# Kernel tuning notes

Measured on AMD Instinct MI355X. Metric: run time of the kernel, lower is better.

The kernel has to match this reference:

```python
import jax, jax.numpy as jnp
import numpy as np

B, C, H, W = 16, 64, 128, 128
E = 8          # number of experts
TOPK = 2       # num_expert (top-k routing)


def setup_inputs() -> dict:
    key = jax.random.key(0)
    ks = jax.random.split(key, 8)
    s = 1.0 / np.sqrt(C)
    x = jax.random.normal(ks[0], (B, C, H, W), dtype=jnp.float32)
    k = jax.random.normal(ks[1], (B, C, 1, 1), dtype=jnp.float32)
    Wg = jax.random.normal(ks[2], (C, E), dtype=jnp.float32) * s
    bg = jnp.zeros((E,), dtype=jnp.float32)
    W1 = jax.random.normal(ks[3], (E, C, C), dtype=jnp.float32) * s  # [E, out, in]
    b1 = jnp.zeros((E, C), dtype=jnp.float32)
    W2 = jax.random.normal(ks[4], (E, C, C), dtype=jnp.float32) * s
    b2 = jnp.zeros((E, C), dtype=jnp.float32)
    return {"x": x, "k": k, "Wg": Wg, "bg": bg, "W1": W1, "b1": b1, "W2": W2, "b2": b2}


def reference(x, k, Wg, bg, W1, b1, W2, b2):
    # --- gate: global avg pool + linear -> [B, E] logits ---
    pooled = x.mean(axis=(2, 3))                              # [B, C]
    logits = pooled @ Wg + bg                                  # [B, E]
    # softmax in fp32 then cast back (matches F.softmax(dtype=torch.float).to(x.dtype))
    weights = jax.nn.softmax(logits.astype(jnp.float32), axis=1).astype(x.dtype)
    topk_w, topk_idx = jax.lax.top_k(weights, TOPK)           # [B, TOPK]
    # scatter top-k weights into dense per-expert mask [B, E]
    mask = jnp.zeros_like(weights).at[jnp.arange(B)[:, None], topk_idx].set(topk_w)
    # --- training branch: run ALL experts, combine with mask ---
    # expert_e(x, k) = W2_e @ gelu((W1_e @ x + b1_e) * k) + b2_e   (1x1 convs)
    h = jnp.einsum('eoc,bchw->ebohw', W1, x) + b1[:, None, :, None, None]
    h = jax.nn.gelu(h * k[None])                               # [E, B, C, H, W]
    y = jnp.einsum('eoc,ebchw->ebohw', W2, h) + b2[:, None, :, None, None]
    out = x + jnp.einsum('ebchw,be->bchw', y, mask)
    return out
```

## Files before the change

kernel.cpp:

```cpp
#include <hip/hip_runtime.h>
#include <hip/hip_bf16.h>


#define BB 16
#define CC 64
#define EE 8
#define HWPX 16384

typedef __bf16 bf16x8 __attribute__((ext_vector_type(8)));
typedef float f32x4 __attribute__((ext_vector_type(4)));

__device__ __forceinline__ unsigned packbf2(float lo, float hi) {
    __bf16 a = (__bf16)lo, b = (__bf16)hi;
    unsigned short ua = __builtin_bit_cast(unsigned short, a);
    unsigned short ub = __builtin_bit_cast(unsigned short, b);
    return ((unsigned)ub << 16) | (unsigned)ua;
}

__device__ __forceinline__ int swz(int px, int d) {
    return px * 32 + ((d & ~3) ^ ((px & 7) << 2)) + (d & 3);
}

__global__ __launch_bounds__(256) void pool_conv_kernel(
    const float* __restrict__ x, float* __restrict__ pooled,
    const float* __restrict__ W1, const float* __restrict__ W2,
    __bf16* __restrict__ W1b, __bf16* __restrict__ W2b) {
    int blk = blockIdx.x;
    if (blk < BB * CC) {
        const float4* p = (const float4*)(x + (size_t)blk * HWPX);
        float s = 0.f;
        for (int i = threadIdx.x; i < HWPX / 4; i += 256) {
            float4 v = p[i];
            s += (v.x + v.y) + (v.z + v.w);
        }
        #pragma unroll
        for (int off = 32; off > 0; off >>= 1) s += __shfl_down(s, off);
        __shared__ float ls[4];
        if ((threadIdx.x & 63) == 0) ls[threadIdx.x >> 6] = s;
        __syncthreads();
        if (threadIdx.x == 0) pooled[blk] = ((ls[0] + ls[1]) + (ls[2] + ls[3])) * (1.0f / (float)HWPX);
    } else {
        int i = (blk - BB * CC) * 256 + threadIdx.x;
        W1b[i] = (__bf16)W1[i];
        W2b[i] = (__bf16)W2[i];
    }
}

__global__ void gate_kernel(const float* __restrict__ pooled,
                            const float* __restrict__ Wg,
                            const float* __restrict__ bg,
                            int* __restrict__ gidx, float* __restrict__ gw) {
    int b = threadIdx.x;
    if (b >= BB) return;
    float logits[EE];
    #pragma unroll
    for (int e = 0; e < EE; ++e) logits[e] = bg[e];
    for (int c = 0; c < CC; ++c) {
        float pv = pooled[b * CC + c];
        #pragma unroll
        for (int e = 0; e < EE; ++e) logits[e] = fmaf(pv, Wg[c * EE + e], logits[e]);
    }
    float m = logits[0];
    #pragma unroll
    for (int e = 1; e < EE; ++e) m = fmaxf(m, logits[e]);
    float w[EE]; float den = 0.f;
    #pragma unroll
    for (int e = 0; e < EE; ++e) { w[e] = expf(logits[e] - m); den += w[e]; }
    float inv = 1.0f / den;
    #pragma unroll
    for (int e = 0; e < EE; ++e) w[e] *= inv;
    int i0 = 0;
    #pragma unroll
    for (int e = 1; e < EE; ++e) if (w[e] > w[i0]) i0 = e;
    int i1 = -1;
    #pragma unroll
    for (int e = 0; e < EE; ++e) {
        if (e == i0) continue;
        if (i1 < 0 || w[e] > w[i1]) i1 = e;
    }
    gidx[b * 2 + 0] = i0; gidx[b * 2 + 1] = i1;
    gw[b * 2 + 0] = w[i0]; gw[b * 2 + 1] = w[i1];
}

__global__ __launch_bounds__(256) void moe_main(
    const float* __restrict__ x, const float* __restrict__ kvec,
    const __bf16* __restrict__ W1b, const float* __restrict__ b1,
    const __bf16* __restrict__ W2b, const float* __restrict__ b2,
    const int* __restrict__ gidx, const float* __restrict__ gw,
    float* __restrict__ out) {

    __shared__ unsigned int lds[2][64 * 32];

    const int blk = blockIdx.x;
    const int b = blk >> 8;
    const int p0 = (blk & 255) << 6;
    const int t = threadIdx.x;
    const int w = t >> 6;
    const int l = t & 63;
    const int g = l >> 4;
    const int l15 = l & 15;

    const int arow = 16 * w + l15;
    const int r0w = 16 * w + 4 * g;

    const int e0 = __builtin_amdgcn_readfirstlane(gidx[b * 2 + 0]);
    const int e1 = __builtin_amdgcn_readfirstlane(gidx[b * 2 + 1]);
    const float wgt0 = gw[b * 2 + 0];
    const float wgt1 = gw[b * 2 + 1];

    bf16x8 a1f[2][2];
    #pragma unroll
    for (int ks = 0; ks < 2; ++ks) {
        a1f[0][ks] = *(const bf16x8*)(W1b + e0 * CC * CC + arow * CC + ks * 32 + g * 8);
        a1f[1][ks] = *(const bf16x8*)(W1b + e1 * CC * CC + arow * CC + ks * 32 + g * 8);
    }
    float b1j[2][4], b2j[2][4], kkj[4];
    #pragma unroll
    for (int j = 0; j < 4; ++j) {
        b1j[0][j] = b1[e0 * CC + r0w + j];
        b1j[1][j] = b1[e1 * CC + r0w + j];
        b2j[0][j] = b2[e0 * CC + r0w + j];
        b2j[1][j] = b2[e1 * CC + r0w + j];
        kkj[j]    = kvec[b * CC + r0w + j];
    }

    {
        const int c0 = (t & 31);
        const int px0 = (t >> 5) * 8;
        const float* r0 = x + ((size_t)(b * CC + c0 * 2)) * HWPX + p0 + px0;
        const float* r1 = r0 + HWPX;
        float4 A0 = *(const float4*)(r0);
        float4 A1 = *(const float4*)(r0 + 4);
        float4 B0 = *(const float4*)(r1);
        float4 B1 = *(const float4*)(r1 + 4);
        float av[8] = {A0.x, A0.y, A0.z, A0.w, A1.x, A1.y, A1.z, A1.w};
        float bv[8] = {B0.x, B0.y, B0.z, B0.w, B1.x, B1.y, B1.z, B1.w};
        #pragma unroll
        for (int i = 0; i < 8; ++i)
            lds[0][swz(px0 + i, c0)] = packbf2(av[i], bv[i]);
    }
    __syncthreads();

    bf16x8 bx[4][2];
    #pragma unroll
    for (int cb = 0; cb < 4; ++cb)
        #pragma unroll
        for (int ks = 0; ks < 2; ++ks)
            bx[cb][ks] = *(const bf16x8*)&lds[0][swz(cb * 16 + l15, ks * 16 + g * 4)];

    const float C1 = -2.302208239f;
    const float C2 = -0.1029434f;

    f32x4 h0[4], h1[4];
    #pragma unroll
    for (int cb = 0; cb < 4; ++cb) {
        h0[cb] = (f32x4){0.f, 0.f, 0.f, 0.f};
        h1[cb] = (f32x4){0.f, 0.f, 0.f, 0.f};
        #pragma unroll
        for (int ks = 0; ks < 2; ++ks) {
            h0[cb] = __builtin_amdgcn_mfma_f32_16x16x32_bf16(a1f[0][ks], bx[cb][ks], h0[cb], 0, 0, 0);
            h1[cb] = __builtin_amdgcn_mfma_f32_16x16x32_bf16(a1f[1][ks], bx[cb][ks], h1[cb], 0, 0, 0);
        }
    }

    uint2 p0k[4], p1k[4];
    #pragma unroll
    for (int cb = 0; cb < 4; ++cb) {
        float hv0[4], hv1[4];
        #pragma unroll
        for (int j = 0; j < 4; ++j) {
            float a0 = h0[cb][j] + b1j[0][j];
            float t0 = a0 * kkj[j];
            float ex0 = __builtin_amdgcn_exp2f(t0 * fmaf(C2, t0 * t0, C1));
            hv0[j] = (t0 * wgt0) * __builtin_amdgcn_rcpf(ex0 + 1.f);
            float a1 = h1[cb][j] + b1j[1][j];
            float t1 = a1 * kkj[j];
            float ex1 = __builtin_amdgcn_exp2f(t1 * fmaf(C2, t1 * t1, C1));
            hv1[j] = (t1 * wgt1) * __builtin_amdgcn_rcpf(ex1 + 1.f);
        }
        p0k[cb].x = packbf2(hv0[0], hv0[1]);
        p0k[cb].y = packbf2(hv0[2], hv0[3]);
        p1k[cb].x = packbf2(hv1[0], hv1[1]);
        p1k[cb].y = packbf2(hv1[2], hv1[3]);
    }

    #pragma unroll
    for (int cb = 0; cb < 4; ++cb)
        *(uint2*)&lds[1][swz(cb * 16 + l15, 8 * w + 2 * g)] = p0k[cb];

    bf16x8 a2f[2][2];
    #pragma unroll
    for (int ks = 0; ks < 2; ++ks) {
        a2f[0][ks] = *(const bf16x8*)(W2b + e0 * CC * CC + arow * CC + ks * 32 + g * 8);
        a2f[1][ks] = *(const bf16x8*)(W2b + e1 * CC * CC + arow * CC + ks * 32 + g * 8);
    }

    __syncthreads();

    #pragma unroll
    for (int cb = 0; cb < 4; ++cb)
        *(uint2*)&lds[0][swz(cb * 16 + l15, 8 * w + 2 * g)] = p1k[cb];

    const float* xbase = x + (size_t)b * CC * HWPX + p0;
    float xp[4][4];
    #pragma unroll
    for (int cb = 0; cb < 4; ++cb)
        #pragma unroll
        for (int j = 0; j < 4; ++j)
            xp[cb][j] = xbase[(size_t)(r0w + j) * HWPX + cb * 16 + l15];

    f32x4 acc2[4];
    #pragma unroll
    for (int cb = 0; cb < 4; ++cb) acc2[cb] = (f32x4){0.f, 0.f, 0.f, 0.f};

    #pragma unroll
    for (int cb = 0; cb < 4; ++cb) {
        #pragma unroll
        for (int ks = 0; ks < 2; ++ks) {
            bf16x8 bh = *(const bf16x8*)&lds[1][swz(cb * 16 + l15, ks * 16 + g * 4)];
            acc2[cb] = __builtin_amdgcn_mfma_f32_16x16x32_bf16(a2f[0][ks], bh, acc2[cb], 0, 0, 0);
        }
    }

    __syncthreads();

    #pragma unroll
    for (int cb = 0; cb < 4; ++cb) {
        #pragma unroll
        for (int ks = 0; ks < 2; ++ks) {
            bf16x8 bh = *(const bf16x8*)&lds[0][swz(cb * 16 + l15, ks * 16 + g * 4)];
            acc2[cb] = __builtin_amdgcn_mfma_f32_16x16x32_bf16(a2f[1][ks], bh, acc2[cb], 0, 0, 0);
        }
    }

    float bsum[4];
    #pragma unroll
    for (int j = 0; j < 4; ++j)
        bsum[j] = fmaf(wgt0, b2j[0][j], wgt1 * b2j[1][j]);

    float* obase = out + (size_t)b * CC * HWPX + p0;
    #pragma unroll
    for (int cb = 0; cb < 4; ++cb) {
        const int col = cb * 16 + l15;
        #pragma unroll
        for (int j = 0; j < 4; ++j) {
            size_t off = (size_t)(r0w + j) * HWPX + col;
            obase[off] = xp[cb][j] + (acc2[cb][j] + bsum[j]);
        }
    }
}

extern "C" void kernel_launch(void* const* d_in, const int* in_sizes, int n_in,
                              void* d_out, int out_size, void* d_ws, size_t ws_size,
                              hipStream_t stream) {
    const float* x  = (const float*)d_in[0];
    const float* k  = (const float*)d_in[1];
    const float* Wg = (const float*)d_in[2];
    const float* bg = (const float*)d_in[3];
    const float* W1 = (const float*)d_in[4];
    const float* b1 = (const float*)d_in[5];
    const float* W2 = (const float*)d_in[6];
    const float* b2 = (const float*)d_in[7];
    float* out = (float*)d_out;

    float*  pooled = (float*)d_ws;
    int*    gidx   = (int*)((char*)d_ws + 4096);
    float*  gw     = (float*)((char*)d_ws + 4096 + 128);
    __bf16* W1b    = (__bf16*)((char*)d_ws + 8192);
    __bf16* W2b    = (__bf16*)((char*)d_ws + 8192 + 65536);

    pool_conv_kernel<<<BB * CC + EE * CC * CC / 256, 256, 0, stream>>>(x, pooled, W1, W2, W1b, W2b);
    gate_kernel<<<1, 64, 0, stream>>>(pooled, Wg, bg, gidx, gw);
    moe_main<<<BB * 256, 256, 0, stream>>>(x, k, W1b, b1, W2b, b2, gidx, gw, out);
}
```

Before: 56.57 us.

## Process four pixel tiles per block with prefetch of next x tile

Each block of moe_main now walks four consecutive 64-pixel tiles instead of one, so the grid shrinks from 4096 to 1024 blocks. Expert weights, biases and k are loaded once per block and reused across the tiles. The next tile's x values are prefetched into registers while the current tile computes. The x tile is now read once per tile (strided per lane) and reused for both the bf16 LDS staging and the residual add, replacing the previous separate vectorized load and reload. The cost is longer-lived registers, more barriers per block, and fewer blocks to hide latency.

New measurement: 51.15 us. 9.6% less time.

```diff
diff --git a/kernel.cpp b/kernel.cpp
--- a/kernel.cpp
+++ b/kernel.cpp
@@ -6,6 +6,7 @@
 #define CC 64
 #define EE 8
 #define HWPX 16384
+#define NT 4
 
 typedef __bf16 bf16x8 __attribute__((ext_vector_type(8)));
 typedef float f32x4 __attribute__((ext_vector_type(4)));
@@ -89,11 +90,12 @@
     const int* __restrict__ gidx, const float* __restrict__ gw,
     float* __restrict__ out) {
 
-    __shared__ unsigned int lds[2][64 * 32];
+    __shared__ unsigned int LA[64 * 32];
+    __shared__ unsigned int LB[64 * 32];
 
     const int blk = blockIdx.x;
-    const int b = blk >> 8;
-    const int p0 = (blk & 255) << 6;
+    const int b = blk >> 6;
+    const int P0 = (blk & 63) << 8;
     const int t = threadIdx.x;
     const int w = t >> 6;
     const int l = t & 63;
@@ -102,150 +104,156 @@
 
     const int arow = 16 * w + l15;
     const int r0w = 16 * w + 4 * g;
+    const int d0 = 8 * w + 2 * g;
 
     const int e0 = __builtin_amdgcn_readfirstlane(gidx[b * 2 + 0]);
     const int e1 = __builtin_amdgcn_readfirstlane(gidx[b * 2 + 1]);
     const float wgt0 = gw[b * 2 + 0];
     const float wgt1 = gw[b * 2 + 1];
 
-    bf16x8 a1f[2][2];
+    const float* xb = x + b * CC * HWPX;
+    float* ob = out + b * CC * HWPX;
+    const int obase = r0w * HWPX + P0 + l15;
+
+    float xc[16];
+    #pragma unroll
+    for (int cb = 0; cb < 4; ++cb)
+        #pragma unroll
+        for (int j = 0; j < 4; ++j)
+            xc[cb * 4 + j] = xb[obase + j * HWPX + cb * 16];
+
+    bf16x8 a1f[2][2], a2f[2][2];
     #pragma unroll
     for (int ks = 0; ks < 2; ++ks) {
         a1f[0][ks] = *(const bf16x8*)(W1b + e0 * CC * CC + arow * CC + ks * 32 + g * 8);
         a1f[1][ks] = *(const bf16x8*)(W1b + e1 * CC * CC + arow * CC + ks * 32 + g * 8);
-    }
-    float b1j[2][4], b2j[2][4], kkj[4];
-    #pragma unroll
-    for (int j = 0; j < 4; ++j) {
-        b1j[0][j] = b1[e0 * CC + r0w + j];
-        b1j[1][j] = b1[e1 * CC + r0w + j];
-        b2j[0][j] = b2[e0 * CC + r0w + j];
-        b2j[1][j] = b2[e1 * CC + r0w + j];
-        kkj[j]    = kvec[b * CC + r0w + j];
-    }
-
-    {
-        const int c0 = (t & 31);
-        const int px0 = (t >> 5) * 8;
-        const float* r0 = x + ((size_t)(b * CC + c0 * 2)) * HWPX + p0 + px0;
-        const float* r1 = r0 + HWPX;
-        float4 A0 = *(const float4*)(r0);
-        float4 A1 = *(const float4*)(r0 + 4);
-        float4 B0 = *(const float4*)(r1);
-        float4 B1 = *(const float4*)(r1 + 4);
-        float av[8] = {A0.x, A0.y, A0.z, A0.w, A1.x, A1.y, A1.z, A1.w};
-        float bv[8] = {B0.x, B0.y, B0.z, B0.w, B1.x, B1.y, B1.z, B1.w};
-        #pragma unroll
-        for (int i = 0; i < 8; ++i)
-            lds[0][swz(px0 + i, c0)] = packbf2(av[i], bv[i]);
-    }
-    __syncthreads();
-
-    bf16x8 bx[4][2];
-    #pragma unroll
-    for (int cb = 0; cb < 4; ++cb)
-        #pragma unroll
-        for (int ks = 0; ks < 2; ++ks)
-            bx[cb][ks] = *(const bf16x8*)&lds[0][swz(cb * 16 + l15, ks * 16 + g * 4)];
+        a2f[0][ks] = *(const bf16x8*)(W2b + e0 * CC * CC + arow * CC + ks * 32 + g * 8);
+        a2f[1][ks] = *(const bf16x8*)(W2b + e1 * CC * CC + arow * CC + ks * 32 + g * 8);
+    }
+    const f32x4 b1v0 = *(const f32x4*)(b1 + e0 * CC + r0w);
+    const f32x4 b1v1 = *(const f32x4*)(b1 + e1 * CC + r0w);
+    const f32x4 b2v0 = *(const f32x4*)(b2 + e0 * CC + r0w);
+    const f32x4 b2v1 = *(const f32x4*)(b2 + e1 * CC + r0w);
+    const f32x4 kk   = *(const f32x4*)(kvec + b * CC + r0w);
+
+    float bsum[4];
+    #pragma unroll
+    for (int j = 0; j < 4; ++j) bsum[j] = fmaf(wgt0, b2v0[j], wgt1 * b2v1[j]);
 
     const float C1 = -2.302208239f;
     const float C2 = -0.1029434f;
 
-    f32x4 h0[4], h1[4];
     #pragma unroll
     for (int cb = 0; cb < 4; ++cb) {
-        h0[cb] = (f32x4){0.f, 0.f, 0.f, 0.f};
-        h1[cb] = (f32x4){0.f, 0.f, 0.f, 0.f};
-        #pragma unroll
-        for (int ks = 0; ks < 2; ++ks) {
-            h0[cb] = __builtin_amdgcn_mfma_f32_16x16x32_bf16(a1f[0][ks], bx[cb][ks], h0[cb], 0, 0, 0);
-            h1[cb] = __builtin_amdgcn_mfma_f32_16x16x32_bf16(a1f[1][ks], bx[cb][ks], h1[cb], 0, 0, 0);
-        }
-    }
-
-    uint2 p0k[4], p1k[4];
-    #pragma unroll
-    for (int cb = 0; cb < 4; ++cb) {
-        float hv0[4], hv1[4];
-        #pragma unroll
-        for (int j = 0; j < 4; ++j) {
-            float a0 = h0[cb][j] + b1j[0][j];
-            float t0 = a0 * kkj[j];
-            float ex0 = __builtin_amdgcn_exp2f(t0 * fmaf(C2, t0 * t0, C1));
-            hv0[j] = (t0 * wgt0) * __builtin_amdgcn_rcpf(ex0 + 1.f);
-            float a1 = h1[cb][j] + b1j[1][j];
-            float t1 = a1 * kkj[j];
-            float ex1 = __builtin_amdgcn_exp2f(t1 * fmaf(C2, t1 * t1, C1));
-            hv1[j] = (t1 * wgt1) * __builtin_amdgcn_rcpf(ex1 + 1.f);
-        }
-        p0k[cb].x = packbf2(hv0[0], hv0[1]);
-        p0k[cb].y = packbf2(hv0[2], hv0[3]);
-        p1k[cb].x = packbf2(hv1[0], hv1[1]);
-        p1k[cb].y = packbf2(hv1[2], hv1[3]);
-    }
-
-    #pragma unroll
-    for (int cb = 0; cb < 4; ++cb)
-        *(uint2*)&lds[1][swz(cb * 16 + l15, 8 * w + 2 * g)] = p0k[cb];
-
-    bf16x8 a2f[2][2];
-    #pragma unroll
-    for (int ks = 0; ks < 2; ++ks) {
-        a2f[0][ks] = *(const bf16x8*)(W2b + e0 * CC * CC + arow * CC + ks * 32 + g * 8);
-        a2f[1][ks] = *(const bf16x8*)(W2b + e1 * CC * CC + arow * CC + ks * 32 + g * 8);
-    }
-
+        uint2 pk;
+        pk.x = packbf2(xc[cb * 4 + 0], xc[cb * 4 + 1]);
+        pk.y = packbf2(xc[cb * 4 + 2], xc[cb * 4 + 3]);
+        *(uint2*)&LA[swz(cb * 16 + l15, d0)] = pk;
+    }
     __syncthreads();
 
     #pragma unroll
-    for (int cb = 0; cb < 4; ++cb)
-        *(uint2*)&lds[0][swz(cb * 16 + l15, 8 * w + 2 * g)] = p1k[cb];
-
-    const float* xbase = x + (size_t)b * CC * HWPX + p0;
-    float xp[4][4];
-    #pragma unroll
-    for (int cb = 0; cb < 4; ++cb)
-        #pragma unroll
-        for (int j = 0; j < 4; ++j)
-            xp[cb][j] = xbase[(size_t)(r0w + j) * HWPX + cb * 16 + l15];
-
-    f32x4 acc2[4];
-    #pragma unroll
-    for (int cb = 0; cb < 4; ++cb) acc2[cb] = (f32x4){0.f, 0.f, 0.f, 0.f};
-
-    #pragma unroll
-    for (int cb = 0; cb < 4; ++cb) {
-        #pragma unroll
-        for (int ks = 0; ks < 2; ++ks) {
-            bf16x8 bh = *(const bf16x8*)&lds[1][swz(cb * 16 + l15, ks * 16 + g * 4)];
-            acc2[cb] = __builtin_amdgcn_mfma_f32_16x16x32_bf16(a2f[0][ks], bh, acc2[cb], 0, 0, 0);
-        }
-    }
-
-    __syncthreads();
-
-    #pragma unroll
-    for (int cb = 0; cb < 4; ++cb) {
-        #pragma unroll
-        for (int ks = 0; ks < 2; ++ks) {
-            bf16x8 bh = *(const bf16x8*)&lds[0][swz(cb * 16 + l15, ks * 16 + g * 4)];
-            acc2[cb] = __builtin_amdgcn_mfma_f32_16x16x32_bf16(a2f[1][ks], bh, acc2[cb], 0, 0, 0);
-        }
-    }
-
-    float bsum[4];
-    #pragma unroll
-    for (int j = 0; j < 4; ++j)
-        bsum[j] = fmaf(wgt0, b2j[0][j], wgt1 * b2j[1][j]);
-
-    float* obase = out + (size_t)b * CC * HWPX + p0;
-    #pragma unroll
-    for (int cb = 0; cb < 4; ++cb) {
-        const int col = cb * 16 + l15;
-        #pragma unroll
-        for (int j = 0; j < 4; ++j) {
-            size_t off = (size_t)(r0w + j) * HWPX + col;
-            obase[off] = xp[cb][j] + (acc2[cb][j] + bsum[j]);
+    for (int it = 0; it < NT; ++it) {
+        unsigned int* XT = (it & 1) ? LB : LA;
+        unsigned int* H0 = (it & 1) ? LA : LB;
+
+        float xn[16];
+        if (it < NT - 1) {
+            #pragma unroll
+            for (int cb = 0; cb < 4; ++cb)
+                #pragma unroll
+                for (int j = 0; j < 4; ++j)
+                    xn[cb * 4 + j] = xb[obase + (it + 1) * 64 + j * HWPX + cb * 16];
+        }
+
+        bf16x8 bx[4][2];
+        #pragma unroll
+        for (int cb = 0; cb < 4; ++cb)
+            #pragma unroll
+            for (int ks = 0; ks < 2; ++ks)
+                bx[cb][ks] = *(const bf16x8*)&XT[swz(cb * 16 + l15, ks * 16 + g * 4)];
+
+        f32x4 h0[4], h1[4];
+        #pragma unroll
+        for (int cb = 0; cb < 4; ++cb) {
+            h0[cb] = (f32x4){0.f, 0.f, 0.f, 0.f};
+            h1[cb] = (f32x4){0.f, 0.f, 0.f, 0.f};
+            #pragma unroll
+            for (int ks = 0; ks < 2; ++ks) {
+                h0[cb] = __builtin_amdgcn_mfma_f32_16x16x32_bf16(a1f[0][ks], bx[cb][ks], h0[cb], 0, 0, 0);
+                h1[cb] = __builtin_amdgcn_mfma_f32_16x16x32_bf16(a1f[1][ks], bx[cb][ks], h1[cb], 0, 0, 0);
+            }
+        }
+
+        uint2 p0k[4], p1k[4];
+        #pragma unroll
+        for (int cb = 0; cb < 4; ++cb) {
+            float hv0[4], hv1[4];
+            #pragma unroll
+            for (int j = 0; j < 4; ++j) {
+                float t0 = (h0[cb][j] + b1v0[j]) * kk[j];
+                float ex0 = __builtin_amdgcn_exp2f(t0 * fmaf(C2, t0 * t0, C1));
+                hv0[j] = (t0 * wgt0) * __builtin_amdgcn_rcpf(ex0 + 1.f);
+                float t1 = (h1[cb][j] + b1v1[j]) * kk[j];
+                float ex1 = __builtin_amdgcn_exp2f(t1 * fmaf(C2, t1 * t1, C1));
+                hv1[j] = (t1 * wgt1) * __builtin_amdgcn_rcpf(ex1 + 1.f);
+            }
+            p0k[cb].x = packbf2(hv0[0], hv0[1]);
+            p0k[cb].y = packbf2(hv0[2], hv0[3]);
+            p1k[cb].x = packbf2(hv1[0], hv1[1]);
+            p1k[cb].y = packbf2(hv1[2], hv1[3]);
+        }
+
+        #pragma unroll
+        for (int cb = 0; cb < 4; ++cb)
+            *(uint2*)&H0[swz(cb * 16 + l15, d0)] = p0k[cb];
+        __syncthreads();
+
+        #pragma unroll
+        for (int cb = 0; cb < 4; ++cb)
+            *(uint2*)&XT[swz(cb * 16 + l15, d0)] = p1k[cb];
+
+        f32x4 acc[4];
+        #pragma unroll
+        for (int cb = 0; cb < 4; ++cb) {
+            acc[cb] = (f32x4){0.f, 0.f, 0.f, 0.f};
+            #pragma unroll
+            for (int ks = 0; ks < 2; ++ks) {
+                bf16x8 bh = *(const bf16x8*)&H0[swz(cb * 16 + l15, ks * 16 + g * 4)];
+                acc[cb] = __builtin_amdgcn_mfma_f32_16x16x32_bf16(a2f[0][ks], bh, acc[cb], 0, 0, 0);
+            }
+        }
+        __syncthreads();
+
+        if (it < NT - 1) {
+            #pragma unroll
+            for (int cb = 0; cb < 4; ++cb) {
+                uint2 pk;
+                pk.x = packbf2(xn[cb * 4 + 0], xn[cb * 4 + 1]);
+                pk.y = packbf2(xn[cb * 4 + 2], xn[cb * 4 + 3]);
+                *(uint2*)&H0[swz(cb * 16 + l15, d0)] = pk;
+            }
+        }
+
+        #pragma unroll
+        for (int cb = 0; cb < 4; ++cb) {
+            #pragma unroll
+            for (int ks = 0; ks < 2; ++ks) {
+                bf16x8 bh = *(const bf16x8*)&XT[swz(cb * 16 + l15, ks * 16 + g * 4)];
+                acc[cb] = __builtin_amdgcn_mfma_f32_16x16x32_bf16(a2f[1][ks], bh, acc[cb], 0, 0, 0);
+            }
+        }
+
+        #pragma unroll
+        for (int cb = 0; cb < 4; ++cb)
+            #pragma unroll
+            for (int j = 0; j < 4; ++j)
+                ob[obase + it * 64 + j * HWPX + cb * 16] = xc[cb * 4 + j] + (acc[cb][j] + bsum[j]);
+
+        if (it < NT - 1) {
+            #pragma unroll
+            for (int i = 0; i < 16; ++i) xc[i] = xn[i];
+            __syncthreads();
         }
     }
 }
@@ -271,5 +279,5 @@
 
     pool_conv_kernel<<<BB * CC + EE * CC * CC / 256, 256, 0, stream>>>(x, pooled, W1, W2, W1b, W2b);
     gate_kernel<<<1, 64, 0, stream>>>(pooled, Wg, bg, gidx, gw);
-    moe_main<<<BB * 256, 256, 0, stream>>>(x, k, W1b, b1, W2b, b2, gidx, gw, out);
-}
+    moe_main<<<BB * 64, 256, 0, stream>>>(x, k, W1b, b1, W2b, b2, gidx, gw, out);
+}
```
